# Kernel optimization log

Hardware: AMD Instinct MI355X
Metric: run time of the kernel (lower is better)

The kernel has to match this reference:

```python
import jax, jax.numpy as jnp
import numpy as np

N = 100000   # nodes
E = 1600000  # edges (avg degree 16)
IN, HID, OUT = 128, 128, 40


def setup_inputs() -> dict:
    key = jax.random.key(0)
    ks = jax.random.split(key, 7)
    return {
        "features": jax.random.normal(ks[0], (N, IN), jnp.float32),
        "src": jax.random.randint(ks[1], (E,), 0, N, jnp.int32),
        "dst": jax.random.randint(ks[2], (E,), 0, N, jnp.int32),
        "W1": jax.random.normal(ks[3], (IN, HID), jnp.float32) / np.sqrt(IN).astype(np.float32),
        "Wh": jax.random.normal(ks[4], (HID, HID), jnp.float32) / np.sqrt(HID).astype(np.float32),
        "W2": jax.random.normal(ks[5], (HID, OUT), jnp.float32) / np.sqrt(HID).astype(np.float32),
        "b2": jnp.zeros((OUT,), jnp.float32),
    }


def _agg(x, src, dst):
    # message passing: gather source node features along edges, sum-scatter to dst
    return jax.ops.segment_sum(x[src], dst, num_segments=N)


def reference(features, src, dst, W1, Wh, W2, b2):
    ones = jnp.ones((E,), jnp.float32)
    out_deg = jnp.clip(jax.ops.segment_sum(ones, src, num_segments=N), 1.0)
    in_deg = jnp.clip(jax.ops.segment_sum(ones, dst, num_segments=N), 1.0)
    lnorm = out_deg[:, None] ** -0.5  # 'both' left norm (src out-degree)
    rnorm = in_deg[:, None] ** -0.5   # 'both' right norm (dst in-degree)

    # conv1: GraphConv(norm='none', bias=False) -> plain sum aggregation, then relu
    h = jax.nn.relu(_agg(features @ W1, src, dst))
    # hidden GraphConv(norm='both', bias=False) + relu (dropout = identity in eval)
    h = jax.nn.relu(_agg((h * lnorm) @ Wh, src, dst) * rnorm)
    # conv2: GraphConv(norm='both', bias=True)
    h = _agg((h * lnorm) @ W2, src, dst) * rnorm + b2
    return jax.nn.log_softmax(h, axis=1)
```

## Files before the change

kernel.cpp:

```cpp
#include <hip/hip_runtime.h>
#include <math.h>

#define MAXDEG 64
#define BCAP 8192
#define EPB 4096

typedef __attribute__((ext_vector_type(8))) short bf16x8;
typedef __attribute__((ext_vector_type(4))) float f32x4;

static __device__ inline unsigned short f2bf(float f) {
    unsigned int u = __float_as_uint(f);
    u += 0x7FFFu + ((u >> 16) & 1u);
    return (unsigned short)(u >> 16);
}
static __device__ inline float bf2f(unsigned short u) {
    return __uint_as_float(((unsigned int)u) << 16);
}
static __device__ inline float4 ld_f4(const float* p) { return *(const float4*)p; }

static __device__ __forceinline__ void acci8(float* a, uint2 u, float s) {
    a[0] += s * (float)((int)(u.x << 24) >> 24);
    a[1] += s * (float)((int)(u.x << 16) >> 24);
    a[2] += s * (float)((int)(u.x << 8) >> 24);
    a[3] += s * (float)((int)u.x >> 24);
    a[4] += s * (float)((int)(u.y << 24) >> 24);
    a[5] += s * (float)((int)(u.y << 16) >> 24);
    a[6] += s * (float)((int)(u.y << 8) >> 24);
    a[7] += s * (float)((int)u.y >> 24);
}

static __global__ __launch_bounds__(256) void wtrans_kernel(
    const float* __restrict__ W1, const float* __restrict__ Wh,
    const float* __restrict__ W2,
    unsigned short* __restrict__ W1t, unsigned short* __restrict__ WhT,
    unsigned short* __restrict__ Wt2) {
    int b = blockIdx.x;
    int t = threadIdx.x;
    if (b == 2) {
        for (int i = t; i < 48 * 128; i += 256) Wt2[i] = 0;
        __syncthreads();
        int n0 = (t & 31) * 4;
        if (n0 < 40) {
            for (int k = t >> 5; k < 128; k += 8) {
                float4 v = ld_f4(&W2[(size_t)k * 40 + n0]);
                Wt2[(size_t)(n0 + 0) * 128 + k] = f2bf(v.x);
                Wt2[(size_t)(n0 + 1) * 128 + k] = f2bf(v.y);
                Wt2[(size_t)(n0 + 2) * 128 + k] = f2bf(v.z);
                Wt2[(size_t)(n0 + 3) * 128 + k] = f2bf(v.w);
            }
        }
        return;
    }
    const float* Wsrc = (b == 0) ? W1 : Wh;
    unsigned short* Wdst = (b == 0) ? W1t : WhT;
    int n0 = (t & 31) * 4;
    for (int k = t >> 5; k < 128; k += 8) {
        float4 v = ld_f4(&Wsrc[(size_t)k * 128 + n0]);
        Wdst[(size_t)(n0 + 0) * 128 + k] = f2bf(v.x);
        Wdst[(size_t)(n0 + 1) * 128 + k] = f2bf(v.y);
        Wdst[(size_t)(n0 + 2) * 128 + k] = f2bf(v.z);
        Wdst[(size_t)(n0 + 3) * 128 + k] = f2bf(v.w);
    }
}

static __device__ __forceinline__ void gemm128_mfma256_q(
    const unsigned short* sa16, const unsigned short* __restrict__ Wt,
    signed char* __restrict__ Y, float* __restrict__ sc,
    int row0, int t, int N) {
    int l = t & 63, w = t >> 6;
    int m = l & 15, kg = l >> 4;
    int row = w * 16 + m;
    int rsw = row & 15;
    f32x4 acc[8];
#pragma unroll
    for (int c = 0; c < 8; ++c) acc[c] = (f32x4){0.f, 0.f, 0.f, 0.f};
#pragma unroll
    for (int ks = 0; ks < 4; ++ks) {
        bf16x8 a = *(const bf16x8*)&sa16[(size_t)row * 128 + (((ks * 4 + kg) ^ rsw) * 8)];
        int kk = ks * 32 + kg * 8;
#pragma unroll
        for (int c = 0; c < 8; ++c) {
            bf16x8 b = *(const bf16x8*)&Wt[(size_t)(c * 16 + m) * 128 + kk];
            acc[c] = __builtin_amdgcn_mfma_f32_16x16x32_bf16(a, b, acc[c], 0, 0, 0);
        }
    }
#pragma unroll
    for (int r = 0; r < 4; ++r) {
        float lm = 0.f;
#pragma unroll
        for (int c = 0; c < 8; ++c) lm = fmaxf(lm, fabsf(acc[c][r]));
#pragma unroll
        for (int o = 1; o < 16; o <<= 1) lm = fmaxf(lm, __shfl_xor(lm, o));
        float inv = lm > 0.f ? 127.f / lm : 0.f;
        int grow = row0 + w * 16 + kg * 4 + r;
        if (grow < N) {
#pragma unroll
            for (int c = 0; c < 8; ++c)
                Y[(size_t)grow * 128 + c * 16 + m] =
                    (signed char)__float2int_rn(acc[c][r] * inv);
            if (m == 0) sc[grow] = lm * (1.f / 127.f);
        }
    }
}

static __device__ __forceinline__ void gemm128_mfma512_q(
    const unsigned short* sa16, const unsigned short* __restrict__ Wt,
    signed char* __restrict__ Y, float* __restrict__ sc,
    unsigned* rmaxu, int row0, int t, int N) {
    int l = t & 63, w = t >> 6;
    int rt = w >> 1, ctb = (w & 1) * 4;
    int m = l & 15, kg = l >> 4;
    int row = rt * 16 + m;
    int rsw = row & 15;
    f32x4 acc[4] = {{0.f, 0.f, 0.f, 0.f}, {0.f, 0.f, 0.f, 0.f},
                    {0.f, 0.f, 0.f, 0.f}, {0.f, 0.f, 0.f, 0.f}};
#pragma unroll
    for (int ks = 0; ks < 4; ++ks) {
        bf16x8 a = *(const bf16x8*)&sa16[(size_t)row * 128 + (((ks * 4 + kg) ^ rsw) * 8)];
        int kk = ks * 32 + kg * 8;
#pragma unroll
        for (int c = 0; c < 4; ++c) {
            int n = (ctb + c) * 16 + m;
            bf16x8 b = *(const bf16x8*)&Wt[(size_t)n * 128 + kk];
            acc[c] = __builtin_amdgcn_mfma_f32_16x16x32_bf16(a, b, acc[c], 0, 0, 0);
        }
    }
#pragma unroll
    for (int r = 0; r < 4; ++r) {
        float lm = 0.f;
#pragma unroll
        for (int c = 0; c < 4; ++c) lm = fmaxf(lm, fabsf(acc[c][r]));
#pragma unroll
        for (int o = 1; o < 16; o <<= 1) lm = fmaxf(lm, __shfl_xor(lm, o));
        if (m == 0)
            atomicMax(&rmaxu[rt * 16 + kg * 4 + r], __float_as_uint(lm));
    }
    __syncthreads();
#pragma unroll
    for (int r = 0; r < 4; ++r) {
        int rl = rt * 16 + kg * 4 + r;
        float am = __uint_as_float(rmaxu[rl]);
        float inv = am > 0.f ? 127.f / am : 0.f;
        int grow = row0 + rl;
        if (grow < N) {
#pragma unroll
            for (int c = 0; c < 4; ++c)
                Y[(size_t)grow * 128 + (ctb + c) * 16 + m] =
                    (signed char)__float2int_rn(acc[c][r] * inv);
            if (ctb == 0 && m == 0) sc[grow] = am * (1.f / 127.f);
        }
    }
}

static __device__ __forceinline__ void gemm40_mfma512(
    const unsigned short* sa16, const unsigned short* __restrict__ Wt2,
    unsigned short* __restrict__ Y3, int row0, int t, int N) {
    int l = t & 63, w = t >> 6;
    int rt = w & 3;
    int nct = (w < 4) ? 2 : 1;
    int ct0 = (w < 4) ? 0 : 2;
    int m = l & 15, kg = l >> 4;
    int row = rt * 16 + m;
    int rsw = row & 15;
    f32x4 acc[2] = {{0.f, 0.f, 0.f, 0.f}, {0.f, 0.f, 0.f, 0.f}};
#pragma unroll
    for (int ks = 0; ks < 4; ++ks) {
        bf16x8 a = *(const bf16x8*)&sa16[(size_t)row * 128 + (((ks * 4 + kg) ^ rsw) * 8)];
        int kk = ks * 32 + kg * 8;
        for (int c = 0; c < nct; ++c) {
            int n = (ct0 + c) * 16 + m;
            bf16x8 b = *(const bf16x8*)&Wt2[(size_t)n * 128 + kk];
            acc[c] = __builtin_amdgcn_mfma_f32_16x16x32_bf16(a, b, acc[c], 0, 0, 0);
        }
    }
    for (int c = 0; c < nct; ++c) {
        int col = (ct0 + c) * 16 + m;
        if (col >= 40) continue;
#pragma unroll
        for (int r = 0; r < 4; ++r) {
            int grow = row0 + rt * 16 + kg * 4 + r;
            if (grow < N) Y3[(size_t)grow * 40 + col] = f2bf(acc[c][r]);
        }
    }
}

template <int MODE>
static __device__ __forceinline__ void gather_phase_i8(
    const signed char* __restrict__ Ysrc, const float* __restrict__ scs,
    unsigned short* sa16,
    const int* __restrict__ csr, const int* __restrict__ indeg,
    const int* __restrict__ outdeg, int row0, int t, int N) {
    int w = t >> 6;
    int l = t & 63;
    int q = l >> 4;
    int lq = l & 15;
    int qb = q * 16;

#pragma unroll
    for (int i = 0; i < 2; ++i) {
        int r = i * 32 + w * 4 + q;
        int node = row0 + r;
        bool valid = node < N;
        int d = 0;
        if (valid) d = indeg[node];
        int dc = d > MAXDEG ? MAXDEG : d;

        int idx0 = 0, idx1 = 0, idx2 = 0, idx3 = 0;
        if (valid) {
            const int* cp = csr + (size_t)node * MAXDEG;
            idx0 = cp[lq];
            if (dc > 16) idx1 = cp[16 + lq];
            if (dc > 32) idx2 = cp[32 + lq];
            if (dc > 48) idx3 = cp[48 + lq];
        }

        float a[8];
#pragma unroll
        for (int x = 0; x < 8; ++x) a[x] = 0.f;

#pragma unroll
        for (int c = 0; c < 4; ++c) {
            int ebase = c * 16;
            if (ebase >= dc) break;
            int v = (c == 0) ? idx0 : (c == 1) ? idx1 : (c == 2) ? idx2 : idx3;
            int lim = dc - ebase;
            if (lim > 16) lim = 16;
            int e = 0;
            for (; e + 4 <= lim; e += 4) {
                int s0 = __shfl(v, qb + e);
                int s1 = __shfl(v, qb + e + 1);
                int s2 = __shfl(v, qb + e + 2);
                int s3 = __shfl(v, qb + e + 3);
                uint2 u0 = *(const uint2*)&Ysrc[(size_t)s0 * 128 + lq * 8];
                uint2 u1 = *(const uint2*)&Ysrc[(size_t)s1 * 128 + lq * 8];
                uint2 u2 = *(const uint2*)&Ysrc[(size_t)s2 * 128 + lq * 8];
                uint2 u3 = *(const uint2*)&Ysrc[(size_t)s3 * 128 + lq * 8];
                float f0 = scs[s0], f1 = scs[s1], f2 = scs[s2], f3 = scs[s3];
                acci8(a, u0, f0); acci8(a, u1, f1);
                acci8(a, u2, f2); acci8(a, u3, f3);
            }
            for (; e < lim; ++e) {
                int s0 = __shfl(v, qb + e);
                uint2 u0 = *(const uint2*)&Ysrc[(size_t)s0 * 128 + lq * 8];
                acci8(a, u0, scs[s0]);
            }
        }

        if (valid) {
            int od = outdeg[node];
            float ln = rsqrtf((float)(od > 1 ? od : 1));
            if (MODE == 0) {
#pragma unroll
                for (int x = 0; x < 8; ++x) a[x] = fmaxf(a[x], 0.f) * ln;
            } else {
                float rn = rsqrtf((float)(d > 1 ? d : 1));
#pragma unroll
                for (int x = 0; x < 8; ++x) a[x] = fmaxf(a[x] * rn, 0.f) * ln;
            }
        }
        uint4 uo;
        uo.x = (unsigned)f2bf(a[0]) | ((unsigned)f2bf(a[1]) << 16);
        uo.y = (unsigned)f2bf(a[2]) | ((unsigned)f2bf(a[3]) << 16);
        uo.z = (unsigned)f2bf(a[4]) | ((unsigned)f2bf(a[5]) << 16);
        uo.w = (unsigned)f2bf(a[6]) | ((unsigned)f2bf(a[7]) << 16);
        int chunk = lq ^ (r & 15);
        *(uint4*)&sa16[(size_t)r * 128 + chunk * 8] = uo;
    }
}

static __global__ __launch_bounds__(256) void bucket_gemm1_kernel(
    const float* __restrict__ A, const unsigned short* __restrict__ W1t,
    signed char* __restrict__ Y, float* __restrict__ s1,
    const int* __restrict__ src, const int* __restrict__ dst,
    int* __restrict__ cntD, int* __restrict__ cntS,
    unsigned int* __restrict__ bktD, unsigned char* __restrict__ bktS,
    int N, int E, int nb, int gG, int gB) {
    __shared__ unsigned short sa16[64 * 128];
    int bid = blockIdx.x;
    int t = threadIdx.x;

    int nI = 5 * gB;
    int role, idx;
    if (bid < nI) {
        if (bid % 5 == 0) { role = 1; idx = bid / 5; }
        else { role = 0; idx = bid - bid / 5 - 1; }
    } else { role = 0; idx = bid - gB; }
    if (role == 1 && idx >= gB) return;
    if (role == 0 && idx >= gG) return;

    if (role == 1) {
        int* sh = (int*)sa16;
        int* hD = sh;
        int* hS = sh + 512;
        int* bD = sh + 1024;
        int* bS = sh + 1536;
        int* cD = sh + 2048;
        int* cS = sh + 2560;
        for (int i = t; i < 512; i += 256) {
            hD[i] = 0; hS[i] = 0; cD[i] = 0; cS[i] = 0;
        }
        __syncthreads();

        int base = idx * EPB + t * 16;
        int s_r[16], d_r[16];
        int nv = 0;
        if (base + 16 <= E) {
            nv = 16;
#pragma unroll
            for (int k = 0; k < 4; ++k) {
                int4 sv = *(const int4*)&src[base + k * 4];
                int4 dv = *(const int4*)&dst[base + k * 4];
                s_r[k * 4 + 0] = sv.x; s_r[k * 4 + 1] = sv.y;
                s_r[k * 4 + 2] = sv.z; s_r[k * 4 + 3] = sv.w;
                d_r[k * 4 + 0] = dv.x; d_r[k * 4 + 1] = dv.y;
                d_r[k * 4 + 2] = dv.z; d_r[k * 4 + 3] = dv.w;
            }
        } else {
            nv = E - base; if (nv < 0) nv = 0; if (nv > 16) nv = 16;
#pragma unroll
            for (int k = 0; k < 16; ++k) {
                if (k < nv) { s_r[k] = src[base + k]; d_r[k] = dst[base + k]; }
                else { s_r[k] = 0; d_r[k] = 0; }
            }
        }

#pragma unroll
        for (int k = 0; k < 16; ++k) {
            if (k < nv) {
                atomicAdd(&hD[d_r[k] >> 8], 1);
                atomicAdd(&hS[s_r[k] >> 8], 1);
            }
        }
        __syncthreads();

        for (int b = t; b < nb; b += 256) {
            int h = hD[b];
            bD[b] = h ? atomicAdd(&cntD[b], h) : 0;
            int h2 = hS[b];
            bS[b] = h2 ? atomicAdd(&cntS[b], h2) : 0;
        }
        __syncthreads();

#pragma unroll
        for (int k = 0; k < 16; ++k) {
            if (k < nv) {
                int d = d_r[k], s = s_r[k];
                int bb = d >> 8;
                int p = atomicAdd(&cD[bb], 1) + bD[bb];
                if (p < BCAP)
                    bktD[(size_t)bb * BCAP + p] =
                        ((unsigned int)(d & 255) << 17) | (unsigned int)s;
                int sb = s >> 8;
                int p2 = atomicAdd(&cS[sb], 1) + bS[sb];
                if (p2 < BCAP)
                    bktS[(size_t)sb * BCAP + p2] = (unsigned char)(s & 255);
            }
        }
        return;
    }

    int row0 = idx * 64;
#pragma unroll
    for (int i = 0; i < 4; ++i) {
        int ci = i * 256 + t;
        int r = ci >> 4;
        int ch = ci & 15;
        int grow = row0 + r;
        uint4 uo = make_uint4(0u, 0u, 0u, 0u);
        if (grow < N) {
            float4 v0 = ld_f4(&A[(size_t)grow * 128 + ch * 8]);
            float4 v1 = ld_f4(&A[(size_t)grow * 128 + ch * 8 + 4]);
            uo.x = (unsigned)f2bf(v0.x) | ((unsigned)f2bf(v0.y) << 16);
            uo.y = (unsigned)f2bf(v0.z) | ((unsigned)f2bf(v0.w) << 16);
            uo.z = (unsigned)f2bf(v1.x) | ((unsigned)f2bf(v1.y) << 16);
            uo.w = (unsigned)f2bf(v1.z) | ((unsigned)f2bf(v1.w) << 16);
        }
        int chunk = ch ^ (r & 15);
        *(uint4*)&sa16[(size_t)r * 128 + chunk * 8] = uo;
    }
    __syncthreads();
    gemm128_mfma256_q(sa16, W1t, Y, s1, row0, t, N);
}

static __global__ __launch_bounds__(256) void csr_build_kernel(
    const int* __restrict__ cntD, const int* __restrict__ cntS,
    const unsigned int* __restrict__ bktD, const unsigned char* __restrict__ bktS,
    int* __restrict__ csr, int* __restrict__ indeg, int* __restrict__ outdeg,
    int N, int nb) {
    __shared__ int cur[256];
    int bid = blockIdx.x;
    int t = threadIdx.x;
    cur[t] = 0;
    __syncthreads();

    if (bid < nb) {
        int b = bid;
        int cnt = cntD[b]; if (cnt > BCAP) cnt = BCAP;
        const unsigned int* bp = bktD + (size_t)b * BCAP;
        for (int i = t; i < cnt; i += 256) {
            unsigned int v = bp[i];
            int d8 = v >> 17;
            int s = (int)(v & 0x1FFFFu);
            int p = atomicAdd(&cur[d8], 1);
            if (p < MAXDEG) csr[((size_t)(b * 256 + d8)) * MAXDEG + p] = s;
        }
        __syncthreads();
        int node = b * 256 + t;
        if (node < N) indeg[node] = cur[t];
    } else {
        int b = bid - nb;
        int cnt = cntS[b]; if (cnt > BCAP) cnt = BCAP;
        const unsigned char* bp = bktS + (size_t)b * BCAP;
        for (int i = t; i < cnt; i += 256) atomicAdd(&cur[bp[i]], 1);
        __syncthreads();
        int node = b * 256 + t;
        if (node < N) outdeg[node] = cur[t];
    }
}

static __global__ __launch_bounds__(512) void agg_gemm2_kernel(
    const signed char* __restrict__ Y1, const float* __restrict__ s1,
    const unsigned short* __restrict__ WhT,
    signed char* __restrict__ Y2, float* __restrict__ s2,
    const int* __restrict__ csr, const int* __restrict__ indeg,
    const int* __restrict__ outdeg, int N) {
    __shared__ unsigned short sa16[64 * 128];
    __shared__ unsigned rmaxu[64];
    int t = threadIdx.x;
    if (t < 64) rmaxu[t] = 0u;
    int row0 = blockIdx.x * 64;
    gather_phase_i8<0>(Y1, s1, sa16, csr, indeg, outdeg, row0, t, N);
    __syncthreads();
    gemm128_mfma512_q(sa16, WhT, Y2, s2, rmaxu, row0, t, N);
}

static __global__ __launch_bounds__(512) void agg_gemm3_kernel(
    const signed char* __restrict__ Y2, const float* __restrict__ s2,
    const unsigned short* __restrict__ Wt2,
    unsigned short* __restrict__ Y3,
    const int* __restrict__ csr, const int* __restrict__ indeg,
    const int* __restrict__ outdeg, int N) {
    __shared__ unsigned short sa16[64 * 128];
    int t = threadIdx.x;
    int row0 = blockIdx.x * 64;
    gather_phase_i8<1>(Y2, s2, sa16, csr, indeg, outdeg, row0, t, N);
    __syncthreads();
    gemm40_mfma512(sa16, Wt2, Y3, row0, t, N);
}

static __global__ __launch_bounds__(512) void agg40_lsm_kernel(
    const unsigned short* __restrict__ Y3, const float* __restrict__ b2,
    const int* __restrict__ csr, const int* __restrict__ indeg,
    float* __restrict__ out, int N) {
    int t = threadIdx.x;
    int node = blockIdx.x * 8 + (t >> 6);
    if (node >= N) return;
    int lane = t & 63;
    int grp = lane >> 4;
    int sub = lane & 15;
    int d = indeg[node];
    int dc = d > MAXDEG ? MAXDEG : d;

    float a0 = 0.f, a1 = 0.f, a2 = 0.f, a3 = 0.f;
    if (sub < 10) {
        const int* cp = csr + (size_t)node * MAXDEG;
        int e = grp;
        for (; e + 12 < dc; e += 16) {
            int s0 = cp[e];
            int s1 = cp[e + 4];
            int s2 = cp[e + 8];
            int s3 = cp[e + 12];
            ushort4 u0 = *(const ushort4*)&Y3[(size_t)s0 * 40 + sub * 4];
            ushort4 u1 = *(const ushort4*)&Y3[(size_t)s1 * 40 + sub * 4];
            ushort4 u2 = *(const ushort4*)&Y3[(size_t)s2 * 40 + sub * 4];
            ushort4 u3 = *(const ushort4*)&Y3[(size_t)s3 * 40 + sub * 4];
            a0 += bf2f(u0.x) + bf2f(u1.x) + bf2f(u2.x) + bf2f(u3.x);
            a1 += bf2f(u0.y) + bf2f(u1.y) + bf2f(u2.y) + bf2f(u3.y);
            a2 += bf2f(u0.z) + bf2f(u1.z) + bf2f(u2.z) + bf2f(u3.z);
            a3 += bf2f(u0.w) + bf2f(u1.w) + bf2f(u2.w) + bf2f(u3.w);
        }
        for (; e < dc; e += 4) {
            int s = cp[e];
            ushort4 u = *(const ushort4*)&Y3[(size_t)s * 40 + sub * 4];
            a0 += bf2f(u.x); a1 += bf2f(u.y); a2 += bf2f(u.z); a3 += bf2f(u.w);
        }
    }
    a0 += __shfl_xor(a0, 16); a0 += __shfl_xor(a0, 32);
    a1 += __shfl_xor(a1, 16); a1 += __shfl_xor(a1, 32);
    a2 += __shfl_xor(a2, 16); a2 += __shfl_xor(a2, 32);
    a3 += __shfl_xor(a3, 16); a3 += __shfl_xor(a3, 32);

    float rs = rsqrtf((float)(d > 1 ? d : 1));
    float x0 = 0.f, x1 = 0.f, x2 = 0.f, x3 = 0.f;
    float mx = -INFINITY;
    if (sub < 10) {
        float4 b = *(const float4*)&b2[sub * 4];
        x0 = a0 * rs + b.x;
        x1 = a1 * rs + b.y;
        x2 = a2 * rs + b.z;
        x3 = a3 * rs + b.w;
        mx = fmaxf(fmaxf(x0, x1), fmaxf(x2, x3));
    }
#pragma unroll
    for (int o = 1; o < 16; o <<= 1) mx = fmaxf(mx, __shfl_xor(mx, o));
    float ex = 0.f;
    if (sub < 10)
        ex = expf(x0 - mx) + expf(x1 - mx) + expf(x2 - mx) + expf(x3 - mx);
#pragma unroll
    for (int o = 1; o < 16; o <<= 1) ex += __shfl_xor(ex, o);
    float ls = logf(ex) + mx;
    if (sub < 10 && grp == 0)
        *(float4*)&out[(size_t)node * 40 + sub * 4] =
            make_float4(x0 - ls, x1 - ls, x2 - ls, x3 - ls);
}


extern "C" void kernel_launch(void* const* d_in, const int* in_sizes, int n_in,
                              void* d_out, int out_size, void* d_ws, size_t ws_size,
                              hipStream_t stream) {
    const float* features = (const float*)d_in[0];
    const int* src = (const int*)d_in[1];
    const int* dst = (const int*)d_in[2];
    const float* W1 = (const float*)d_in[3];
    const float* Wh = (const float*)d_in[4];
    const float* W2 = (const float*)d_in[5];
    const float* b2 = (const float*)d_in[6];
    float* out = (float*)d_out;

    const int N = in_sizes[0] / 128;
    const int E = in_sizes[1];
    const int nb = (N + 255) / 256;

    char* p = (char*)d_ws;
    auto carve = [&](size_t bytes) {
        char* q = p;
        p += (bytes + 255) & ~(size_t)255;
        return q;
    };
    signed char* bufY1 = (signed char*)carve((size_t)N * 128);
    float* sc1 = (float*)carve((size_t)N * 4);
    signed char* bufY2 = (signed char*)carve((size_t)N * 128);
    float* sc2 = (float*)carve((size_t)N * 4);
    unsigned short* bufY3 = (unsigned short*)carve((size_t)N * 40 * 2);
    int* csr = (int*)carve((size_t)N * MAXDEG * 4);
    unsigned int* bktD = (unsigned int*)carve((size_t)nb * BCAP * 4);
    unsigned char* bktS = (unsigned char*)carve((size_t)nb * BCAP);
    int* cntD = (int*)carve((size_t)nb * 4);
    int* cntS = (int*)carve((size_t)nb * 4);
    int* indeg = (int*)carve((size_t)N * 4);
    int* outdeg = (int*)carve((size_t)N * 4);
    unsigned short* W1t = (unsigned short*)carve((size_t)128 * 128 * 2);
    unsigned short* WhT = (unsigned short*)carve((size_t)128 * 128 * 2);
    unsigned short* Wt2 = (unsigned short*)carve((size_t)48 * 128 * 2);
    (void)ws_size; (void)n_in; (void)out_size;

    hipMemsetAsync(cntD, 0, (size_t)nb * 4, stream);
    hipMemsetAsync(cntS, 0, (size_t)nb * 4, stream);

    int gG = (N + 63) / 64;
    int gB = (E + EPB - 1) / EPB;
    wtrans_kernel<<<3, 256, 0, stream>>>(W1, Wh, W2, W1t, WhT, Wt2);
    bucket_gemm1_kernel<<<gG + gB, 256, 0, stream>>>(
        features, W1t, bufY1, sc1, src, dst, cntD, cntS, bktD, bktS,
        N, E, nb, gG, gB);
    csr_build_kernel<<<2 * nb, 256, 0, stream>>>(
        cntD, cntS, bktD, bktS, csr, indeg, outdeg, N, nb);
    agg_gemm2_kernel<<<gG, 512, 0, stream>>>(bufY1, sc1, WhT, bufY2, sc2,
                                             csr, indeg, outdeg, N);
    agg_gemm3_kernel<<<gG, 512, 0, stream>>>(bufY2, sc2, Wt2, bufY3,
                                             csr, indeg, outdeg, N);
    agg40_lsm_kernel<<<(N + 7) / 8, 512, 0, stream>>>(bufY3, b2, csr, indeg, out, N);
}
```

Before: 270.3 us.

## Store activations as offset-biased uint8 and gather 16 bytes per lane

Stores quantized activations as unsigned bytes biased by 128, so the gather can unpack with masks and shifts instead of sign-extension. The bias is removed once per row by subtracting 128 times the summed scales. Each lane now loads 16 bytes per edge and processes two edges per step, using half-wave groups that are merged with a shuffle-xor. Per-neighbour scales are prefetched alongside the CSR indices and broadcast by shuffle rather than reloaded for every element. This cuts per-edge load instruction count and ALU work, at the cost of more registers and a cross-lane reduction.

```diff
diff --git a/kernel.cpp b/kernel.cpp
--- a/kernel.cpp
+++ b/kernel.cpp
@@ -18,15 +18,23 @@
 }
 static __device__ inline float4 ld_f4(const float* p) { return *(const float4*)p; }
 
-static __device__ __forceinline__ void acci8(float* a, uint2 u, float s) {
-    a[0] += s * (float)((int)(u.x << 24) >> 24);
-    a[1] += s * (float)((int)(u.x << 16) >> 24);
-    a[2] += s * (float)((int)(u.x << 8) >> 24);
-    a[3] += s * (float)((int)u.x >> 24);
-    a[4] += s * (float)((int)(u.y << 24) >> 24);
-    a[5] += s * (float)((int)(u.y << 16) >> 24);
-    a[6] += s * (float)((int)(u.y << 8) >> 24);
-    a[7] += s * (float)((int)u.y >> 24);
+static __device__ __forceinline__ void accu16(float* a, uint4 u, float f) {
+    a[0]  += f * (float)(u.x & 0xffu);
+    a[1]  += f * (float)((u.x >> 8) & 0xffu);
+    a[2]  += f * (float)((u.x >> 16) & 0xffu);
+    a[3]  += f * (float)(u.x >> 24);
+    a[4]  += f * (float)(u.y & 0xffu);
+    a[5]  += f * (float)((u.y >> 8) & 0xffu);
+    a[6]  += f * (float)((u.y >> 16) & 0xffu);
+    a[7]  += f * (float)(u.y >> 24);
+    a[8]  += f * (float)(u.z & 0xffu);
+    a[9]  += f * (float)((u.z >> 8) & 0xffu);
+    a[10] += f * (float)((u.z >> 16) & 0xffu);
+    a[11] += f * (float)(u.z >> 24);
+    a[12] += f * (float)(u.w & 0xffu);
+    a[13] += f * (float)((u.w >> 8) & 0xffu);
+    a[14] += f * (float)((u.w >> 16) & 0xffu);
+    a[15] += f * (float)(u.w >> 24);
 }
 
 static __global__ __launch_bounds__(256) void wtrans_kernel(
@@ -65,7 +73,7 @@
 
 static __device__ __forceinline__ void gemm128_mfma256_q(
     const unsigned short* sa16, const unsigned short* __restrict__ Wt,
-    signed char* __restrict__ Y, float* __restrict__ sc,
+    unsigned char* __restrict__ Y, float* __restrict__ sc,
     int row0, int t, int N) {
     int l = t & 63, w = t >> 6;
     int m = l & 15, kg = l >> 4;
@@ -97,7 +105,7 @@
 #pragma unroll
             for (int c = 0; c < 8; ++c)
                 Y[(size_t)grow * 128 + c * 16 + m] =
-                    (signed char)__float2int_rn(acc[c][r] * inv);
+                    (unsigned char)(__float2int_rn(acc[c][r] * inv) + 128);
             if (m == 0) sc[grow] = lm * (1.f / 127.f);
         }
     }
@@ -105,7 +113,7 @@
 
 static __device__ __forceinline__ void gemm128_mfma512_q(
     const unsigned short* sa16, const unsigned short* __restrict__ Wt,
-    signed char* __restrict__ Y, float* __restrict__ sc,
+    unsigned char* __restrict__ Y, float* __restrict__ sc,
     unsigned* rmaxu, int row0, int t, int N) {
     int l = t & 63, w = t >> 6;
     int rt = w >> 1, ctb = (w & 1) * 4;
@@ -146,7 +154,7 @@
 #pragma unroll
             for (int c = 0; c < 4; ++c)
                 Y[(size_t)grow * 128 + (ctb + c) * 16 + m] =
-                    (signed char)__float2int_rn(acc[c][r] * inv);
+                    (unsigned char)(__float2int_rn(acc[c][r] * inv) + 128);
             if (ctb == 0 && m == 0) sc[grow] = am * (1.f / 127.f);
         }
     }
@@ -185,8 +193,8 @@
 }
 
 template <int MODE>
-static __device__ __forceinline__ void gather_phase_i8(
-    const signed char* __restrict__ Ysrc, const float* __restrict__ scs,
+static __device__ __forceinline__ void gather_phase_u8(
+    const unsigned char* __restrict__ Ysrc, const float* __restrict__ scs,
     unsigned short* sa16,
     const int* __restrict__ csr, const int* __restrict__ indeg,
     const int* __restrict__ outdeg, int row0, int t, int N) {
@@ -195,6 +203,8 @@
     int q = l >> 4;
     int lq = l & 15;
     int qb = q * 16;
+    int oct = lq >> 3;
+    int ol = lq & 7;
 
 #pragma unroll
     for (int i = 0; i < 2; ++i) {
@@ -206,71 +216,80 @@
         int dc = d > MAXDEG ? MAXDEG : d;
 
         int idx0 = 0, idx1 = 0, idx2 = 0, idx3 = 0;
+        float sc0 = 0.f, sc1 = 0.f, sc2 = 0.f, sc3 = 0.f;
         if (valid) {
             const int* cp = csr + (size_t)node * MAXDEG;
-            idx0 = cp[lq];
-            if (dc > 16) idx1 = cp[16 + lq];
-            if (dc > 32) idx2 = cp[32 + lq];
-            if (dc > 48) idx3 = cp[48 + lq];
-        }
-
-        float a[8];
-#pragma unroll
-        for (int x = 0; x < 8; ++x) a[x] = 0.f;
+            if (lq < dc)      { idx0 = cp[lq];      sc0 = scs[idx0]; }
+            if (lq + 16 < dc) { idx1 = cp[lq + 16]; sc1 = scs[idx1]; }
+            if (lq + 32 < dc) { idx2 = cp[lq + 32]; sc2 = scs[idx2]; }
+            if (lq + 48 < dc) { idx3 = cp[lq + 48]; sc3 = scs[idx3]; }
+        }
+
+        float a[16];
+#pragma unroll
+        for (int x = 0; x < 16; ++x) a[x] = 0.f;
+        float S = 0.f;
 
 #pragma unroll
         for (int c = 0; c < 4; ++c) {
             int ebase = c * 16;
             if (ebase >= dc) break;
             int v = (c == 0) ? idx0 : (c == 1) ? idx1 : (c == 2) ? idx2 : idx3;
+            float vs = (c == 0) ? sc0 : (c == 1) ? sc1 : (c == 2) ? sc2 : sc3;
             int lim = dc - ebase;
             if (lim > 16) lim = 16;
-            int e = 0;
-            for (; e + 4 <= lim; e += 4) {
-                int s0 = __shfl(v, qb + e);
-                int s1 = __shfl(v, qb + e + 1);
-                int s2 = __shfl(v, qb + e + 2);
-                int s3 = __shfl(v, qb + e + 3);
-                uint2 u0 = *(const uint2*)&Ysrc[(size_t)s0 * 128 + lq * 8];
-                uint2 u1 = *(const uint2*)&Ysrc[(size_t)s1 * 128 + lq * 8];
-                uint2 u2 = *(const uint2*)&Ysrc[(size_t)s2 * 128 + lq * 8];
-                uint2 u3 = *(const uint2*)&Ysrc[(size_t)s3 * 128 + lq * 8];
-                float f0 = scs[s0], f1 = scs[s1], f2 = scs[s2], f3 = scs[s3];
-                acci8(a, u0, f0); acci8(a, u1, f1);
-                acci8(a, u2, f2); acci8(a, u3, f3);
-            }
-            for (; e < lim; ++e) {
-                int s0 = __shfl(v, qb + e);
-                uint2 u0 = *(const uint2*)&Ysrc[(size_t)s0 * 128 + lq * 8];
-                acci8(a, u0, scs[s0]);
-            }
-        }
+            for (int e = 0; e < lim; e += 2) {
+                int s = __shfl(v, qb + e + oct);
+                float f = __shfl(vs, qb + e + oct);
+                uint4 u = *(const uint4*)&Ysrc[(size_t)s * 128 + ol * 16];
+                S += f;
+                accu16(a, u, f);
+            }
+        }
+
+#pragma unroll
+        for (int x = 0; x < 16; ++x) a[x] += __shfl_xor(a[x], 8);
+        S += __shfl_xor(S, 8);
 
         if (valid) {
+            float bias = 128.f * S;
             int od = outdeg[node];
             float ln = rsqrtf((float)(od > 1 ? od : 1));
             if (MODE == 0) {
 #pragma unroll
-                for (int x = 0; x < 8; ++x) a[x] = fmaxf(a[x], 0.f) * ln;
+                for (int x = 0; x < 16; ++x)
+                    a[x] = fmaxf(a[x] - bias, 0.f) * ln;
             } else {
                 float rn = rsqrtf((float)(d > 1 ? d : 1));
 #pragma unroll
-                for (int x = 0; x < 8; ++x) a[x] = fmaxf(a[x] * rn, 0.f) * ln;
-            }
-        }
+                for (int x = 0; x < 16; ++x)
+                    a[x] = fmaxf((a[x] - bias) * rn, 0.f) * ln;
+            }
+        } else {
+#pragma unroll
+            for (int x = 0; x < 16; ++x) a[x] = 0.f;
+        }
+
         uint4 uo;
-        uo.x = (unsigned)f2bf(a[0]) | ((unsigned)f2bf(a[1]) << 16);
-        uo.y = (unsigned)f2bf(a[2]) | ((unsigned)f2bf(a[3]) << 16);
-        uo.z = (unsigned)f2bf(a[4]) | ((unsigned)f2bf(a[5]) << 16);
-        uo.w = (unsigned)f2bf(a[6]) | ((unsigned)f2bf(a[7]) << 16);
-        int chunk = lq ^ (r & 15);
+        if (oct == 0) {
+            uo.x = (unsigned)f2bf(a[0]) | ((unsigned)f2bf(a[1]) << 16);
+            uo.y = (unsigned)f2bf(a[2]) | ((unsigned)f2bf(a[3]) << 16);
+            uo.z = (unsigned)f2bf(a[4]) | ((unsigned)f2bf(a[5]) << 16);
+            uo.w = (unsigned)f2bf(a[6]) | ((unsigned)f2bf(a[7]) << 16);
+        } else {
+            uo.x = (unsigned)f2bf(a[8]) | ((unsigned)f2bf(a[9]) << 16);
+            uo.y = (unsigned)f2bf(a[10]) | ((unsigned)f2bf(a[11]) << 16);
+            uo.z = (unsigned)f2bf(a[12]) | ((unsigned)f2bf(a[13]) << 16);
+            uo.w = (unsigned)f2bf(a[14]) | ((unsigned)f2bf(a[15]) << 16);
+        }
+        int chunk = (2 * ol + oct) ^ (r & 15);
         *(uint4*)&sa16[(size_t)r * 128 + chunk * 8] = uo;
     }
 }
 
 static __global__ __launch_bounds__(256) void bucket_gemm1_kernel(
     const float* __restrict__ A, const unsigned short* __restrict__ W1t,
-    signed char* __restrict__ Y, float* __restrict__ s1,
+    unsigned char* __restrict__ Y, float* __restrict__ s1,
     const int* __restrict__ src, const int* __restrict__ dst,
     int* __restrict__ cntD, int* __restrict__ cntS,
     unsigned int* __restrict__ bktD, unsigned char* __restrict__ bktS,
@@ -419,9 +438,9 @@
 }
 
 static __global__ __launch_bounds__(512) void agg_gemm2_kernel(
-    const signed char* __restrict__ Y1, const float* __restrict__ s1,
+    const unsigned char* __restrict__ Y1, const float* __restrict__ s1,
     const unsigned short* __restrict__ WhT,
-    signed char* __restrict__ Y2, float* __restrict__ s2,
+    unsigned char* __restrict__ Y2, float* __restrict__ s2,
     const int* __restrict__ csr, const int* __restrict__ indeg,
     const int* __restrict__ outdeg, int N) {
     __shared__ unsigned short sa16[64 * 128];
@@ -429,13 +448,13 @@
     int t = threadIdx.x;
     if (t < 64) rmaxu[t] = 0u;
     int row0 = blockIdx.x * 64;
-    gather_phase_i8<0>(Y1, s1, sa16, csr, indeg, outdeg, row0, t, N);
+    gather_phase_u8<0>(Y1, s1, sa16, csr, indeg, outdeg, row0, t, N);
     __syncthreads();
     gemm128_mfma512_q(sa16, WhT, Y2, s2, rmaxu, row0, t, N);
 }
 
 static __global__ __launch_bounds__(512) void agg_gemm3_kernel(
-    const signed char* __restrict__ Y2, const float* __restrict__ s2,
+    const unsigned char* __restrict__ Y2, const float* __restrict__ s2,
     const unsigned short* __restrict__ Wt2,
     unsigned short* __restrict__ Y3,
     const int* __restrict__ csr, const int* __restrict__ indeg,
@@ -443,7 +462,7 @@
     __shared__ unsigned short sa16[64 * 128];
     int t = threadIdx.x;
     int row0 = blockIdx.x * 64;
-    gather_phase_i8<1>(Y2, s2, sa16, csr, indeg, outdeg, row0, t, N);
+    gather_phase_u8<1>(Y2, s2, sa16, csr, indeg, outdeg, row0, t, N);
     __syncthreads();
     gemm40_mfma512(sa16, Wt2, Y3, row0, t, N);
 }
@@ -537,9 +556,9 @@
         p += (bytes + 255) & ~(size_t)255;
         return q;
     };
-    signed char* bufY1 = (signed char*)carve((size_t)N * 128);
+    unsigned char* bufY1 = (unsigned char*)carve((size_t)N * 128);
     float* sc1 = (float*)carve((size_t)N * 4);
-    signed char* bufY2 = (signed char*)carve((size_t)N * 128);
+    unsigned char* bufY2 = (unsigned char*)carve((size_t)N * 128);
     float* sc2 = (float*)carve((size_t)N * 4);
     unsigned short* bufY3 = (unsigned short*)carve((size_t)N * 40 * 2);
     int* csr = (int*)carve((size_t)N * MAXDEG * 4);
```

Result: slower. 287.0 us (+6.2%).
